# Kernel optimization log

Hardware: AMD Instinct MI355X
Metric: run time of the kernel (lower is better)

## Reference

```python
import jax, jax.numpy as jnp
import numpy as np

N_NODES = 150000
N_USERS = 100000
EMB = 64
N_EDGES = 4800000
N_LAYERS = 3


def setup_inputs() -> dict:
    key = jax.random.key(0)
    k1, k2, k3, k4 = jax.random.split(key, 4)
    emb_weight = jax.random.normal(k1, (N_NODES, EMB), dtype=jnp.float32)
    adj_row = jnp.sort(jax.random.randint(k2, (N_EDGES,), 0, N_NODES, dtype=jnp.int64))
    adj_col = jax.random.randint(k3, (N_EDGES,), 0, N_NODES, dtype=jnp.int64)
    adj_vals = jax.random.uniform(k4, (N_EDGES,), dtype=jnp.float32)
    return {
        "emb_weight": emb_weight,
        "adj_row": adj_row,
        "adj_col": adj_col,
        "adj_vals": adj_vals,
        "n_users": N_USERS,
        "n_nodes": N_NODES,
        "n_layers": N_LAYERS,
    }


def _spmm(row, col, vals, x, n_nodes):
    # COO SpMM: out[r] += vals[e] * x[col[e]]  for each edge e with row[e]==r
    gathered = x[col] * vals[:, None]            # [nnz, emb]
    return jax.ops.segment_sum(gathered, row, num_segments=n_nodes)


def reference(emb_weight, adj_row, adj_col, adj_vals, n_users, n_nodes, n_layers):
    all_emb = emb_weight
    embs_sum = all_emb                           # running sum instead of stack+mean
    for _ in range(n_layers):
        all_emb = _spmm(adj_row, adj_col, adj_vals, all_emb, n_nodes)
        embs_sum = embs_sum + all_emb
    final_emb = embs_sum / jnp.asarray(n_layers + 1, dtype=emb_weight.dtype)
    users = final_emb[:n_users]
    items = final_emb[n_users:]
    return (users, items)
```

## Files before the change

### kernel.cpp

```cpp
#include <hip/hip_runtime.h>

#define EMB 64

__device__ __forceinline__ float bl(unsigned int u) { return __uint_as_float(u << 16); }
__device__ __forceinline__ float bh(unsigned int u) { return __uint_as_float(u & 0xffff0000u); }
__device__ __forceinline__ unsigned int pack2(float a, float b) {
    unsigned int ua = __float_as_uint(a); ua += 0x7fffu + ((ua >> 16) & 1u);
    unsigned int ub = __float_as_uint(b); ub += 0x7fffu + ((ub >> 16) & 1u);
    return (ua >> 16) | (ub & 0xffff0000u);
}

__global__ void __launch_bounds__(256) k_rowptr(const int* __restrict__ row,
                                                int* __restrict__ ptr, int E, int R) {
    int e = blockIdx.x * blockDim.x + threadIdx.x;
    if (e >= E) return;
    int r = row[e];
    int prev = (e == 0) ? -1 : row[e - 1];
    for (int q = prev + 1; q <= r; ++q) ptr[q] = e;
    if (e == E - 1) {
        for (int q = r + 1; q <= R; ++q) ptr[q] = E;
    }
}

__global__ void __launch_bounds__(256) k_prep(const float* __restrict__ emb,
                                              float* __restrict__ sum,
                                              uint4* __restrict__ Xb, int n8) {
    int i = blockIdx.x * blockDim.x + threadIdx.x;
    if (i >= n8) return;
    const float4* p = reinterpret_cast<const float4*>(emb) + (size_t)i * 2;
    float4 a = p[0], b = p[1];
    float4* sp = reinterpret_cast<float4*>(sum) + (size_t)i * 2;
    sp[0] = a; sp[1] = b;
    uint4 x;
    x.x = pack2(a.x, a.y); x.y = pack2(a.z, a.w);
    x.z = pack2(b.x, b.y); x.w = pack2(b.z, b.w);
    Xb[i] = x;
}

template <int FINAL>
__global__ void __launch_bounds__(256) k_spmm(const int* __restrict__ ptr,
                                              const int* __restrict__ col,
                                              const float* __restrict__ vals,
                                              const uint4* __restrict__ Xb,
                                              uint4* __restrict__ Yb,
                                              float* __restrict__ SUM, int R) {
    int tid = blockIdx.x * blockDim.x + threadIdx.x;
    int g   = tid >> 3;
    int gl  = tid & 7;
    if (g >= R) return;

    int s = ptr[g];
    int e = ptr[g + 1];

    float acc0 = 0.f, acc1 = 0.f, acc2 = 0.f, acc3 = 0.f;
    float acc4 = 0.f, acc5 = 0.f, acc6 = 0.f, acc7 = 0.f;

    for (int base = s; base < e; base += 8) {
        int n = min(8, e - base);
        int   c = 0;
        float v = 0.f;
        if (gl < n) {
            c = col[base + gl];
            v = vals[base + gl];
        }
        if (n == 8) {
            int   cj[8];
            float vj[8];
            #pragma unroll
            for (int j = 0; j < 8; ++j) {
                cj[j] = __shfl(c, j, 8);
                vj[j] = __shfl(v, j, 8);
            }
            uint4 xv[8];
            #pragma unroll
            for (int j = 0; j < 8; ++j)
                xv[j] = Xb[(size_t)cj[j] * 8 + gl];
            #pragma unroll
            for (int j = 0; j < 8; ++j) {
                acc0 = fmaf(vj[j], bl(xv[j].x), acc0);
                acc1 = fmaf(vj[j], bh(xv[j].x), acc1);
                acc2 = fmaf(vj[j], bl(xv[j].y), acc2);
                acc3 = fmaf(vj[j], bh(xv[j].y), acc3);
                acc4 = fmaf(vj[j], bl(xv[j].z), acc4);
                acc5 = fmaf(vj[j], bh(xv[j].z), acc5);
                acc6 = fmaf(vj[j], bl(xv[j].w), acc6);
                acc7 = fmaf(vj[j], bh(xv[j].w), acc7);
            }
        } else {
            for (int j = 0; j < n; ++j) {
                int   cjj = __shfl(c, j, 8);
                float vjs = __shfl(v, j, 8);
                uint4 xv  = Xb[(size_t)cjj * 8 + gl];
                acc0 = fmaf(vjs, bl(xv.x), acc0);
                acc1 = fmaf(vjs, bh(xv.x), acc1);
                acc2 = fmaf(vjs, bl(xv.y), acc2);
                acc3 = fmaf(vjs, bh(xv.y), acc3);
                acc4 = fmaf(vjs, bl(xv.z), acc4);
                acc5 = fmaf(vjs, bh(xv.z), acc5);
                acc6 = fmaf(vjs, bl(xv.w), acc6);
                acc7 = fmaf(vjs, bh(xv.w), acc7);
            }
        }
    }

    float4* sp = reinterpret_cast<float4*>(SUM + (size_t)g * EMB + gl * 8);
    float4 a = sp[0], b = sp[1];
    if (FINAL) {
        a.x = (a.x + acc0) * 0.25f; a.y = (a.y + acc1) * 0.25f;
        a.z = (a.z + acc2) * 0.25f; a.w = (a.w + acc3) * 0.25f;
        b.x = (b.x + acc4) * 0.25f; b.y = (b.y + acc5) * 0.25f;
        b.z = (b.z + acc6) * 0.25f; b.w = (b.w + acc7) * 0.25f;
        sp[0] = a; sp[1] = b;
    } else {
        a.x += acc0; a.y += acc1; a.z += acc2; a.w += acc3;
        b.x += acc4; b.y += acc5; b.z += acc6; b.w += acc7;
        sp[0] = a; sp[1] = b;
        uint4 y;
        y.x = pack2(acc0, acc1); y.y = pack2(acc2, acc3);
        y.z = pack2(acc4, acc5); y.w = pack2(acc6, acc7);
        Yb[(size_t)g * 8 + gl] = y;
    }
}

extern "C" void kernel_launch(void* const* d_in, const int* in_sizes, int n_in,
                              void* d_out, int out_size, void* d_ws, size_t ws_size,
                              hipStream_t stream) {
    const float* emb  = (const float*)d_in[0];
    const int*   row  = (const int*)d_in[1];
    const int*   col  = (const int*)d_in[2];
    const float* vals = (const float*)d_in[3];

    int nemb = in_sizes[0];
    int E    = in_sizes[1];
    int R    = nemb / EMB;

    uint4* X0  = (uint4*)d_ws;
    uint4* X1  = X0 + nemb / 8;
    int*   ptr = (int*)(X1 + nemb / 8);
    float* SUM = (float*)d_out;

    dim3 blk(256);
    int gridE    = (E + 255) / 256;
    int gridPrep = (nemb / 8 + 255) / 256;
    int gridRows = (R * 8 + 255) / 256;

    k_rowptr<<<gridE, blk, 0, stream>>>(row, ptr, E, R);
    k_prep<<<gridPrep, blk, 0, stream>>>(emb, SUM, X0, nemb / 8);

    k_spmm<0><<<gridRows, blk, 0, stream>>>(ptr, col, vals, X0, X1, SUM, R);
    k_spmm<0><<<gridRows, blk, 0, stream>>>(ptr, col, vals, X1, X0, SUM, R);
    k_spmm<1><<<gridRows, blk, 0, stream>>>(ptr, col, vals, X0, X1, SUM, R);
}
```

Before: 344.2 us.

## Keep layer outputs in bf16 buffers and sum them in a final pass

The SpMM kernel no longer reads and writes the fp32 running sum on every layer. Each layer's bf16 output now goes into its own buffer, and one final elementwise kernel adds the fp32 input to the three bf16 layers and scales by a quarter. The edge loop now handles 16 edges per iteration, prefetches the next chunk's col/val indices before the FMAs, and clamps indices so there is no separate tail path. Rows with no edges exit early with zeros. The cost is more workspace, one extra launch, and a final sum built from bf16-rounded layer outputs rather than fp32 accumulation, plus higher register use from the 16-wide unroll.

```diff
diff --git a/kernel.cpp b/kernel.cpp
--- a/kernel.cpp
+++ b/kernel.cpp
@@ -23,27 +23,30 @@
 }
 
 __global__ void __launch_bounds__(256) k_prep(const float* __restrict__ emb,
-                                              float* __restrict__ sum,
                                               uint4* __restrict__ Xb, int n8) {
     int i = blockIdx.x * blockDim.x + threadIdx.x;
     if (i >= n8) return;
     const float4* p = reinterpret_cast<const float4*>(emb) + (size_t)i * 2;
     float4 a = p[0], b = p[1];
-    float4* sp = reinterpret_cast<float4*>(sum) + (size_t)i * 2;
-    sp[0] = a; sp[1] = b;
     uint4 x;
     x.x = pack2(a.x, a.y); x.y = pack2(a.z, a.w);
     x.z = pack2(b.x, b.y); x.w = pack2(b.z, b.w);
     Xb[i] = x;
 }
 
-template <int FINAL>
+__device__ __forceinline__ void loadcv(const int* __restrict__ col,
+                                       const float* __restrict__ vals,
+                                       int idx, int lim, int& c, float& v) {
+    int i = idx < lim ? idx : lim - 1;
+    c = col[i];
+    v = (idx < lim) ? vals[i] : 0.f;
+}
+
 __global__ void __launch_bounds__(256) k_spmm(const int* __restrict__ ptr,
                                               const int* __restrict__ col,
                                               const float* __restrict__ vals,
                                               const uint4* __restrict__ Xb,
-                                              uint4* __restrict__ Yb,
-                                              float* __restrict__ SUM, int R) {
+                                              uint4* __restrict__ Yb, int R) {
     int tid = blockIdx.x * blockDim.x + threadIdx.x;
     int g   = tid >> 3;
     int gl  = tid & 7;
@@ -52,74 +55,78 @@
     int s = ptr[g];
     int e = ptr[g + 1];
 
+    if (s >= e) {
+        Yb[(size_t)g * 8 + gl] = make_uint4(0u, 0u, 0u, 0u);
+        return;
+    }
+
     float acc0 = 0.f, acc1 = 0.f, acc2 = 0.f, acc3 = 0.f;
     float acc4 = 0.f, acc5 = 0.f, acc6 = 0.f, acc7 = 0.f;
 
-    for (int base = s; base < e; base += 8) {
-        int n = min(8, e - base);
-        int   c = 0;
-        float v = 0.f;
-        if (gl < n) {
-            c = col[base + gl];
-            v = vals[base + gl];
+    int   c0, c1;
+    float v0, v1;
+    loadcv(col, vals, s + gl,     e, c0, v0);
+    loadcv(col, vals, s + 8 + gl, e, c1, v1);
+
+    for (int base = s; base < e; base += 16) {
+        int   cj[16];
+        float vj[16];
+        #pragma unroll
+        for (int j = 0; j < 8; ++j) {
+            cj[j]     = __shfl(c0, j, 8);
+            vj[j]     = __shfl(v0, j, 8);
+            cj[8 + j] = __shfl(c1, j, 8);
+            vj[8 + j] = __shfl(v1, j, 8);
         }
-        if (n == 8) {
-            int   cj[8];
-            float vj[8];
-            #pragma unroll
-            for (int j = 0; j < 8; ++j) {
-                cj[j] = __shfl(c, j, 8);
-                vj[j] = __shfl(v, j, 8);
-            }
-            uint4 xv[8];
-            #pragma unroll
-            for (int j = 0; j < 8; ++j)
-                xv[j] = Xb[(size_t)cj[j] * 8 + gl];
-            #pragma unroll
-            for (int j = 0; j < 8; ++j) {
-                acc0 = fmaf(vj[j], bl(xv[j].x), acc0);
-                acc1 = fmaf(vj[j], bh(xv[j].x), acc1);
-                acc2 = fmaf(vj[j], bl(xv[j].y), acc2);
-                acc3 = fmaf(vj[j], bh(xv[j].y), acc3);
-                acc4 = fmaf(vj[j], bl(xv[j].z), acc4);
-                acc5 = fmaf(vj[j], bh(xv[j].z), acc5);
-                acc6 = fmaf(vj[j], bl(xv[j].w), acc6);
-                acc7 = fmaf(vj[j], bh(xv[j].w), acc7);
-            }
-        } else {
-            for (int j = 0; j < n; ++j) {
-                int   cjj = __shfl(c, j, 8);
-                float vjs = __shfl(v, j, 8);
-                uint4 xv  = Xb[(size_t)cjj * 8 + gl];
-                acc0 = fmaf(vjs, bl(xv.x), acc0);
-                acc1 = fmaf(vjs, bh(xv.x), acc1);
-                acc2 = fmaf(vjs, bl(xv.y), acc2);
-                acc3 = fmaf(vjs, bh(xv.y), acc3);
-                acc4 = fmaf(vjs, bl(xv.z), acc4);
-                acc5 = fmaf(vjs, bh(xv.z), acc5);
-                acc6 = fmaf(vjs, bl(xv.w), acc6);
-                acc7 = fmaf(vjs, bh(xv.w), acc7);
-            }
+        uint4 xv[16];
+        #pragma unroll
+        for (int j = 0; j < 16; ++j)
+            xv[j] = Xb[(size_t)cj[j] * 8 + gl];
+        int nbase = base + 16;
+        if (nbase < e) {
+            loadcv(col, vals, nbase + gl,     e, c0, v0);
+            loadcv(col, vals, nbase + 8 + gl, e, c1, v1);
+        }
+        #pragma unroll
+        for (int j = 0; j < 16; ++j) {
+            acc0 = fmaf(vj[j], bl(xv[j].x), acc0);
+            acc1 = fmaf(vj[j], bh(xv[j].x), acc1);
+            acc2 = fmaf(vj[j], bl(xv[j].y), acc2);
+            acc3 = fmaf(vj[j], bh(xv[j].y), acc3);
+            acc4 = fmaf(vj[j], bl(xv[j].z), acc4);
+            acc5 = fmaf(vj[j], bh(xv[j].z), acc5);
+            acc6 = fmaf(vj[j], bl(xv[j].w), acc6);
+            acc7 = fmaf(vj[j], bh(xv[j].w), acc7);
         }
     }
 
-    float4* sp = reinterpret_cast<float4*>(SUM + (size_t)g * EMB + gl * 8);
-    float4 a = sp[0], b = sp[1];
-    if (FINAL) {
-        a.x = (a.x + acc0) * 0.25f; a.y = (a.y + acc1) * 0.25f;
-        a.z = (a.z + acc2) * 0.25f; a.w = (a.w + acc3) * 0.25f;
-        b.x = (b.x + acc4) * 0.25f; b.y = (b.y + acc5) * 0.25f;
-        b.z = (b.z + acc6) * 0.25f; b.w = (b.w + acc7) * 0.25f;
-        sp[0] = a; sp[1] = b;
-    } else {
-        a.x += acc0; a.y += acc1; a.z += acc2; a.w += acc3;
-        b.x += acc4; b.y += acc5; b.z += acc6; b.w += acc7;
-        sp[0] = a; sp[1] = b;
-        uint4 y;
-        y.x = pack2(acc0, acc1); y.y = pack2(acc2, acc3);
-        y.z = pack2(acc4, acc5); y.w = pack2(acc6, acc7);
-        Yb[(size_t)g * 8 + gl] = y;
-    }
+    uint4 y;
+    y.x = pack2(acc0, acc1); y.y = pack2(acc2, acc3);
+    y.z = pack2(acc4, acc5); y.w = pack2(acc6, acc7);
+    Yb[(size_t)g * 8 + gl] = y;
+}
+
+__global__ void __launch_bounds__(256) k_final(const float* __restrict__ emb,
+                                               const uint4* __restrict__ X1,
+                                               const uint4* __restrict__ X2,
+                                               const uint4* __restrict__ X3,
+                                               float* __restrict__ out, int n8) {
+    int i = blockIdx.x * blockDim.x + threadIdx.x;
+    if (i >= n8) return;
+    const float4* p = reinterpret_cast<const float4*>(emb) + (size_t)i * 2;
+    float4 a = p[0], b = p[1];
+    uint4 x1 = X1[i], x2 = X2[i], x3 = X3[i];
+    float4 o0, o1;
+    o0.x = 0.25f * (a.x + bl(x1.x) + bl(x2.x) + bl(x3.x));
+    o0.y = 0.25f * (a.y + bh(x1.x) + bh(x2.x) + bh(x3.x));
+    o0.z = 0.25f * (a.z + bl(x1.y) + bl(x2.y) + bl(x3.y));
+    o0.w = 0.25f * (a.w + bh(x1.y) + bh(x2.y) + bh(x3.y));
+    o1.x = 0.25f * (b.x + bl(x1.z) + bl(x2.z) + bl(x3.z));
+    o1.y = 0.25f * (b.y + bh(x1.z) + bh(x2.z) + bh(x3.z));
+    o1.z = 0.25f * (b.z + bl(x1.w) + bl(x2.w) + bl(x3.w));
+    o1.w = 0.25f * (b.w + bh(x1.w) + bh(x2.w) + bh(x3.w));
+    float4* q = reinterpret_cast<float4*>(out) + (size_t)i * 2;
+    q[0] = o0; q[1] = o1;
 }
 
 extern "C" void kernel_launch(void* const* d_in, const int* in_sizes, int n_in,
@@ -136,18 +143,21 @@
 
     uint4* X0  = (uint4*)d_ws;
     uint4* X1  = X0 + nemb / 8;
-    int*   ptr = (int*)(X1 + nemb / 8);
-    float* SUM = (float*)d_out;
+    uint4* X2  = X1 + nemb / 8;
+    uint4* X3  = X2 + nemb / 8;
+    int*   ptr = (int*)(X3 + nemb / 8);
 
     dim3 blk(256);
     int gridE    = (E + 255) / 256;
-    int gridPrep = (nemb / 8 + 255) / 256;
+    int gridElem = (nemb / 8 + 255) / 256;
     int gridRows = (R * 8 + 255) / 256;
 
     k_rowptr<<<gridE, blk, 0, stream>>>(row, ptr, E, R);
-    k_prep<<<gridPrep, blk, 0, stream>>>(emb, SUM, X0, nemb / 8);
+    k_prep<<<gridElem, blk, 0, stream>>>(emb, X0, nemb / 8);
 
-    k_spmm<0><<<gridRows, blk, 0, stream>>>(ptr, col, vals, X0, X1, SUM, R);
-    k_spmm<0><<<gridRows, blk, 0, stream>>>(ptr, col, vals, X1, X0, SUM, R);
-    k_spmm<1><<<gridRows, blk, 0, stream>>>(ptr, col, vals, X0, X1, SUM, R);
+    k_spmm<<<gridRows, blk, 0, stream>>>(ptr, col, vals, X0, X1, R);
+    k_spmm<<<gridRows, blk, 0, stream>>>(ptr, col, vals, X1, X2, R);
+    k_spmm<<<gridRows, blk, 0, stream>>>(ptr, col, vals, X2, X3, R);
+
+    k_final<<<gridElem, blk, 0, stream>>>(emb, X1, X2, X3, (float*)d_out, nemb / 8);
 }
```

Measured after the change: 280.7 us. -18.4%, faster.
